# Kernel tuning notes

Hardware: AMD Instinct MI355X
Metric: run time of the kernel (lower is better)

The kernel has to match this reference:

```python
import jax, jax.numpy as jnp
import numpy as np

D_MODEL = 1024
N_HEADS = 16
DEPTH = D_MODEL // N_HEADS
D_FF = 4096
B, S = 2, 2048
EPS = 1e-5


def _layernorm(x, g, b):
    mu = jnp.mean(x, axis=-1, keepdims=True)
    var = jnp.mean(jnp.square(x - mu), axis=-1, keepdims=True)
    return (x - mu) * jax.lax.rsqrt(var + EPS) * g + b


def setup_inputs() -> dict:
    key = jax.random.key(0)
    ks = jax.random.split(key, 16)
    sd = 0.02
    d = {
        'x': jax.random.normal(ks[0], (B, S, D_MODEL), dtype=jnp.float32),
        'mask': jnp.ones((B, S), dtype=jnp.int32),
        'wq_w': jax.random.normal(ks[1], (D_MODEL, D_MODEL), dtype=jnp.float32) * sd,
        'wq_b': jnp.zeros((D_MODEL,), dtype=jnp.float32),
        'wk_w': jax.random.normal(ks[2], (D_MODEL, D_MODEL), dtype=jnp.float32) * sd,
        'wk_b': jnp.zeros((D_MODEL,), dtype=jnp.float32),
        'wv_w': jax.random.normal(ks[3], (D_MODEL, D_MODEL), dtype=jnp.float32) * sd,
        'wv_b': jnp.zeros((D_MODEL,), dtype=jnp.float32),
        'wo_w': jax.random.normal(ks[4], (D_MODEL, D_MODEL), dtype=jnp.float32) * sd,
        'wo_b': jnp.zeros((D_MODEL,), dtype=jnp.float32),
        'ffn_w1': jax.random.normal(ks[5], (D_MODEL, D_FF), dtype=jnp.float32) * sd,
        'ffn_b1': jnp.zeros((D_FF,), dtype=jnp.float32),
        'ffn_w2': jax.random.normal(ks[6], (D_FF, D_MODEL), dtype=jnp.float32) * sd,
        'ffn_b2': jnp.zeros((D_MODEL,), dtype=jnp.float32),
        'ln1_g': jnp.ones((D_MODEL,), dtype=jnp.float32),
        'ln1_b': jnp.zeros((D_MODEL,), dtype=jnp.float32),
        'ln2_g': jnp.ones((D_MODEL,), dtype=jnp.float32),
        'ln2_b': jnp.zeros((D_MODEL,), dtype=jnp.float32),
    }
    return d


def reference(x, mask, wq_w, wq_b, wk_w, wk_b, wv_w, wv_b, wo_w, wo_b,
              ffn_w1, ffn_b1, ffn_w2, ffn_b2, ln1_g, ln1_b, ln2_g, ln2_b):
    b, s, _ = x.shape
    # projections [B,S,D] -> [B,H,S,depth]
    def split_heads(t):
        return t.reshape(b, s, N_HEADS, DEPTH).transpose(0, 2, 1, 3)
    q = split_heads(x @ wq_w + wq_b)
    k = split_heads(x @ wk_w + wk_b)
    v = split_heads(x @ wv_w + wv_b)
    # scores [B,H,S,S]
    logits = jnp.einsum('bhqd,bhkd->bhqk', q, k) / jnp.sqrt(jnp.float32(DEPTH))
    m = mask[:, None, None, :]  # [B,1,1,S] broadcast over heads/query
    logits = jnp.where(m == 0, jnp.float32(-1e9), logits)
    attn = jax.nn.softmax(logits, axis=-1)
    ctx = jnp.einsum('bhqk,bhkd->bhqd', attn, v)
    ctx = ctx.transpose(0, 2, 1, 3).reshape(b, s, D_MODEL)
    attn_out = ctx @ wo_w + wo_b
    out1 = _layernorm(x + attn_out, ln1_g, ln1_b)
    ffn = jax.nn.relu(out1 @ ffn_w1 + ffn_b1) @ ffn_w2 + ffn_b2
    out2 = _layernorm(out1 + ffn, ln2_g, ln2_b)
    return out2
```

## Files before the change

kernel.cpp:

```cpp
#include <hip/hip_runtime.h>
#include <hip/hip_bf16.h>

#define D_MODEL 1024
#define N_HEADS 16
#define DEPTH   64
#define D_FF    4096
#define BATCH   2
#define SEQ     2048
#define NTOK    (BATCH * SEQ)
#define EPS     1e-5f

typedef __attribute__((ext_vector_type(8))) short short8;
typedef __attribute__((ext_vector_type(4))) float f32x4;
typedef __attribute__((ext_vector_type(4))) unsigned short ushort4v;
typedef __attribute__((ext_vector_type(8))) unsigned short ushort8v;

__device__ __forceinline__ unsigned short f2bf(float f) {
    union { __hip_bfloat16 h; unsigned short u; } cv;
    cv.h = __float2bfloat16(f);
    return cv.u;
}

__device__ __forceinline__ float bf2f(unsigned short u) {
    union { float f; unsigned int i; } c;
    c.i = (unsigned int)u << 16;
    return c.f;
}

__device__ __forceinline__ float exp2_fast(float x) {
    float r;
    asm("v_exp_f32 %0, %1" : "=v"(r) : "v"(x));
    return r;
}

__device__ __forceinline__ void gload16(const unsigned short* g, unsigned short* lds) {
    __builtin_amdgcn_global_load_lds(
        (const __attribute__((address_space(1))) void*)g,
        (__attribute__((address_space(3))) void*)lds, 16, 0, 0);
}

__device__ __forceinline__ void tc_tile(
    const float* __restrict__ W, unsigned short* __restrict__ WT,
    int K, int N, int bn64, int bk64, int tid, float (*t)[65])
{
    const int bk = bk64 * 64, bn = bn64 * 64;
    const int c4 = tid & 15, r0 = tid >> 4;
#pragma unroll
    for (int i = 0; i < 4; ++i) {
        int k = r0 + i * 16;
        f32x4 v = *(const f32x4*)&W[(size_t)(bk + k) * N + bn + c4 * 4];
#pragma unroll
        for (int jj = 0; jj < 4; ++jj) t[k][c4 * 4 + jj] = v[jj];
    }
    __syncthreads();
#pragma unroll
    for (int i = 0; i < 4; ++i) {
        int n = r0 + i * 16;
        ushort4v o;
#pragma unroll
        for (int jj = 0; jj < 4; ++jj) o[jj] = f2bf(t[c4 * 4 + jj][n]);
        *(ushort4v*)&WT[(size_t)(bn + n) * K + bk + c4 * 4] = o;
    }
}

__global__ __launch_bounds__(256) void prep_kernel(
    const float* __restrict__ wq_w, const float* __restrict__ wk_w,
    const float* __restrict__ wv_w, const float* __restrict__ wo_w,
    const float* __restrict__ ffn_w1, const float* __restrict__ ffn_w2,
    const float* __restrict__ wq_b, const float* __restrict__ wk_b,
    const float* __restrict__ wv_b, const float* __restrict__ x,
    unsigned short* __restrict__ wqkvT, unsigned short* __restrict__ woT,
    unsigned short* __restrict__ w1T, unsigned short* __restrict__ w2T,
    float* __restrict__ biasqkv, unsigned short* __restrict__ actb)
{
    __shared__ float t[64][65];
    const int idx = blockIdx.x, tid = threadIdx.x;

    if (idx < 1024) {
        const int wsel = idx >> 8, rel = idx & 255;
        const float* W = (wsel == 0) ? wq_w : (wsel == 1) ? wk_w : (wsel == 2) ? wv_w : wo_w;
        unsigned short* WT = (wsel == 3) ? woT : (wqkvT + (size_t)wsel * 1024 * 1024);
        tc_tile(W, WT, 1024, 1024, rel & 15, rel >> 4, tid, t);
    } else if (idx < 2048) {
        const int rel = idx - 1024;
        tc_tile(ffn_w1, w1T, 1024, 4096, rel & 63, rel >> 6, tid, t);
    } else if (idx < 3072) {
        const int rel = idx - 2048;
        tc_tile(ffn_w2, w2T, 4096, 1024, rel & 15, rel >> 4, tid, t);
    } else if (idx < 3084) {
        const int i = (idx - 3072) * 256 + tid;
        if (i < 1024) biasqkv[i] = wq_b[i];
        else if (i < 2048) biasqkv[i] = wk_b[i - 1024];
        else if (i < 3072) biasqkv[i] = wv_b[i - 2048];
    } else {
        const int i = ((idx - 3084) * 256 + tid) * 8;
        f32x4 a = *(const f32x4*)&x[i];
        f32x4 b = *(const f32x4*)&x[i + 4];
        ushort8v o;
        o[0] = f2bf(a[0]); o[1] = f2bf(a[1]); o[2] = f2bf(a[2]); o[3] = f2bf(a[3]);
        o[4] = f2bf(b[0]); o[5] = f2bf(b[1]); o[6] = f2bf(b[2]); o[7] = f2bf(b[3]);
        *(ushort8v*)&actb[i] = o;
    }
}

__global__ __launch_bounds__(256) void vtrans_kernel(
    const unsigned short* __restrict__ QKV, unsigned short* __restrict__ Vt)
{
    __shared__ unsigned short T[64][72];
    const int st = blockIdx.x * 64;
    const int h = blockIdx.y, b = blockIdx.z;
    const int tid = threadIdx.x;
    const size_t tok0 = (size_t)b * SEQ;
    const int LD = 3 * D_MODEL;
    const int r = tid >> 3, c8 = (tid & 7) * 8;
#pragma unroll
    for (int p = 0; p < 2; ++p) {
        int row = p * 32 + r;
        *(ushort8v*)&T[row][c8] =
            *(const ushort8v*)&QKV[(tok0 + st + row) * LD + 2048 + h * 64 + c8];
    }
    __syncthreads();
    const int bh = b * N_HEADS + h;
#pragma unroll
    for (int p = 0; p < 2; ++p) {
        int d = p * 32 + r;
        ushort8v o;
#pragma unroll
        for (int e = 0; e < 8; ++e) o[e] = T[c8 + e][d];
        *(ushort8v*)&Vt[((size_t)bh * 64 + d) * SEQ + st + c8] = o;
    }
}

__global__ __launch_bounds__(512, 2) void gemm256_kernel(
    const unsigned short* __restrict__ A, const unsigned short* __restrict__ BT,
    const float* __restrict__ bias, float* __restrict__ C,
    unsigned short* __restrict__ Cb,
    int M, int N, int lda, int kLen, int ksplit, int relu, int out_bf)
{
    __shared__ unsigned short As[2][256 * 64];
    __shared__ unsigned short Bs[2][256 * 64];
    const int tid = threadIdx.x;
    const int lane = tid & 63, w = tid >> 6;
    const int wr = w >> 2, wc = w & 3;
    const int lr = lane & 15, g = lane >> 4;

    const int nwg = gridDim.x;
    int wg = blockIdx.x;
    if ((nwg & 7) == 0) wg = (wg & 7) * (nwg >> 3) + (wg >> 3);
    if (ksplit > 1) {
        const int ntile = nwg / ksplit;
        const int split = wg / ntile;
        wg = wg % ntile;
        A  += (size_t)split * kLen;
        BT += (size_t)split * kLen;
        C  += (size_t)split * M * N;
        Cb += (size_t)split * M * N;
    }
    const int gx = N >> 8;
    const int bm = (wg / gx) * 256, bn = (wg % gx) * 256;

    const int srow = (w << 3) + (lane >> 3);
    const int scol = ((lane & 7) ^ (lane >> 3)) << 3;
    const int ldst = (w << 9);

#define STG(P, Xs, bufi, hf, rb, k0)                                            \
    {                                                                            \
        gload16(P + (size_t)((rb) + (hf) * 128 + srow) * lda + (k0) + scol,      \
                &Xs[bufi][(hf) * 8192 + ldst]);                                  \
        gload16(P + (size_t)((rb) + (hf) * 128 + 64 + srow) * lda + (k0) + scol, \
                &Xs[bufi][(hf) * 8192 + 4096 + ldst]);                           \
    }

    const int NS = kLen >> 6;
    f32x4 acc[8][4] = {};

    STG(A,  As, 0, 0, bm, 0); STG(A,  As, 0, 1, bm, 0);
    STG(BT, Bs, 0, 0, bn, 0); STG(BT, Bs, 0, 1, bn, 0);
    if (NS > 1) { STG(BT, Bs, 1, 0, bn, 64); STG(BT, Bs, 1, 1, bn, 64); }
    asm volatile("s_waitcnt vmcnt(4)" ::: "memory");
    __builtin_amdgcn_s_barrier();
    asm volatile("" ::: "memory");

    int buf = 0;
    short8 af[4][2], b0[2][2], b1[2][2];
    for (int s = 0; s < NS; ++s) {
        const int kn1 = (s + 1) << 6, kn2 = (s + 2) << 6;

#pragma unroll
        for (int i = 0; i < 4; ++i)
#pragma unroll
            for (int kk = 0; kk < 2; ++kk)
                af[i][kk] = *(const short8*)&As[buf][(wr * 128 + i * 16 + lr) * 64
                                                    + (((kk * 4 + g) ^ (lr & 7)) << 3)];
#pragma unroll
        for (int j = 0; j < 2; ++j)
#pragma unroll
            for (int kk = 0; kk < 2; ++kk)
                b0[j][kk] = *(const short8*)&Bs[buf][(wc * 64 + j * 16 + lr) * 64
                                                    + (((kk * 4 + g) ^ (lr & 7)) << 3)];
        if (s + 1 < NS) STG(A, As, buf ^ 1, 0, bm, kn1);
        asm volatile("" ::: "memory");
        __builtin_amdgcn_s_barrier();
        asm volatile("" ::: "memory");
        __builtin_amdgcn_s_setprio(1);
#pragma unroll
        for (int i = 0; i < 4; ++i)
#pragma unroll
            for (int j = 0; j < 2; ++j) {
                acc[i][j] = __builtin_amdgcn_mfma_f32_16x16x32_bf16(af[i][0], b0[j][0], acc[i][j], 0, 0, 0);
                acc[i][j] = __builtin_amdgcn_mfma_f32_16x16x32_bf16(af[i][1], b0[j][1], acc[i][j], 0, 0, 0);
            }
        __builtin_amdgcn_s_setprio(0);
        asm volatile("" ::: "memory");
        __builtin_amdgcn_s_barrier();
        asm volatile("" ::: "memory");

#pragma unroll
        for (int j = 0; j < 2; ++j)
#pragma unroll
            for (int kk = 0; kk < 2; ++kk)
                b1[j][kk] = *(const short8*)&Bs[buf][(wc * 64 + (j + 2) * 16 + lr) * 64
                                                    + (((kk * 4 + g) ^ (lr & 7)) << 3)];
        if (s + 1 < NS) STG(A, As, buf ^ 1, 1, bm, kn1);
        asm volatile("" ::: "memory");
        __builtin_amdgcn_s_barrier();
        asm volatile("" ::: "memory");
        __builtin_amdgcn_s_setprio(1);
#pragma unroll
        for (int i = 0; i < 4; ++i)
#pragma unroll
            for (int j = 0; j < 2; ++j) {
                acc[i][j + 2] = __builtin_amdgcn_mfma_f32_16x16x32_bf16(af[i][0], b1[j][0], acc[i][j + 2], 0, 0, 0);
                acc[i][j + 2] = __builtin_amdgcn_mfma_f32_16x16x32_bf16(af[i][1], b1[j][1], acc[i][j + 2], 0, 0, 0);
            }
        __builtin_amdgcn_s_setprio(0);
        asm volatile("" ::: "memory");
        __builtin_amdgcn_s_barrier();
        asm volatile("" ::: "memory");

#pragma unroll
        for (int i = 0; i < 4; ++i)
#pragma unroll
            for (int kk = 0; kk < 2; ++kk)
                af[i][kk] = *(const short8*)&As[buf][(wr * 128 + 64 + i * 16 + lr) * 64
                                                    + (((kk * 4 + g) ^ (lr & 7)) << 3)];
        if (s + 2 < NS) STG(BT, Bs, buf, 0, bn, kn2);
        asm volatile("" ::: "memory");
        __builtin_amdgcn_s_barrier();
        asm volatile("" ::: "memory");
        __builtin_amdgcn_s_setprio(1);
#pragma unroll
        for (int i = 0; i < 4; ++i)
#pragma unroll
            for (int j = 0; j < 2; ++j) {
                acc[i + 4][j] = __builtin_amdgcn_mfma_f32_16x16x32_bf16(af[i][0], b0[j][0], acc[i + 4][j], 0, 0, 0);
                acc[i + 4][j] = __builtin_amdgcn_mfma_f32_16x16x32_bf16(af[i][1], b0[j][1], acc[i + 4][j], 0, 0, 0);
            }
        __builtin_amdgcn_s_setprio(0);
        asm volatile("" ::: "memory");
        __builtin_amdgcn_s_barrier();
        asm volatile("" ::: "memory");

        if (s + 2 < NS) STG(BT, Bs, buf, 1, bn, kn2);
        asm volatile("" ::: "memory");
        __builtin_amdgcn_s_barrier();
        asm volatile("" ::: "memory");
        __builtin_amdgcn_s_setprio(1);
#pragma unroll
        for (int i = 0; i < 4; ++i)
#pragma unroll
            for (int j = 0; j < 2; ++j) {
                acc[i + 4][j + 2] = __builtin_amdgcn_mfma_f32_16x16x32_bf16(af[i][0], b1[j][0], acc[i + 4][j + 2], 0, 0, 0);
                acc[i + 4][j + 2] = __builtin_amdgcn_mfma_f32_16x16x32_bf16(af[i][1], b1[j][1], acc[i + 4][j + 2], 0, 0, 0);
            }
        __builtin_amdgcn_s_setprio(0);
        asm volatile("s_waitcnt vmcnt(4)" ::: "memory");
        __builtin_amdgcn_s_barrier();
        asm volatile("" ::: "memory");

        buf ^= 1;
    }
#undef STG

#pragma unroll
    for (int i = 0; i < 8; ++i)
#pragma unroll
        for (int j = 0; j < 4; ++j) {
            const int col = bn + wc * 64 + j * 16 + lr;
            const float bv = bias ? bias[col] : 0.f;
#pragma unroll
            for (int r = 0; r < 4; ++r) {
                const int row = bm + wr * 128 + i * 16 + g * 4 + r;
                float v = acc[i][j][r] + bv;
                if (relu) v = fmaxf(v, 0.f);
                if (out_bf) Cb[(size_t)row * N + col] = f2bf(v);
                else        C [(size_t)row * N + col] = v;
            }
        }
}

__global__ __launch_bounds__(256) void gemm_bt_kernel(
    const unsigned short* __restrict__ A, const unsigned short* __restrict__ BT,
    const float* __restrict__ bias, float* __restrict__ C,
    unsigned short* __restrict__ Cb,
    int M, int N, int lda, int kLen, int relu, int out_bf)
{
    __shared__ unsigned short As[128 * 64];
    __shared__ unsigned short Bs[128 * 64];
    const int tid = threadIdx.x;
    const int lane = tid & 63, wv = tid >> 6;
    const int wr = wv >> 1, wc = wv & 1;
    const int bm = blockIdx.y * 128, bn = blockIdx.x * 128;
    const int kbase = blockIdx.z * kLen;
    const int lr = lane & 15, lk = (lane >> 4) << 3;

    C  += (size_t)blockIdx.z * M * N;
    Cb += (size_t)blockIdx.z * M * N;

    f32x4 acc[4][4] = {};

    for (int kt = 0; kt < kLen; kt += 64) {
#pragma unroll
        for (int c = 0; c < 4; ++c) {
            int e = c * 2048 + tid * 8;
            int row = e >> 6, k = e & 63;
            gload16(A  + (size_t)(bm + row) * lda + kbase + kt + k, As + c * 2048 + wv * 512);
            gload16(BT + (size_t)(bn + row) * lda + kbase + kt + k, Bs + c * 2048 + wv * 512);
        }
        __syncthreads();
#pragma unroll
        for (int kk = 0; kk < 2; ++kk) {
            short8 af[4], bfr[4];
#pragma unroll
            for (int i = 0; i < 4; ++i) {
                af[i]  = *(const short8*)&As[(wr * 64 + i * 16 + lr) * 64 + kk * 32 + lk];
                bfr[i] = *(const short8*)&Bs[(wc * 64 + i * 16 + lr) * 64 + kk * 32 + lk];
            }
#pragma unroll
            for (int i = 0; i < 4; ++i)
#pragma unroll
                for (int j = 0; j < 4; ++j)
                    acc[i][j] = __builtin_amdgcn_mfma_f32_16x16x32_bf16(
                        af[i], bfr[j], acc[i][j], 0, 0, 0);
        }
        __syncthreads();
    }

    const int r0 = bm + wr * 64, c0 = bn + wc * 64;
    const int rq = (lane >> 4) * 4;
#pragma unroll
    for (int i = 0; i < 4; ++i)
#pragma unroll
        for (int j = 0; j < 4; ++j) {
            int col = c0 + j * 16 + lr;
            float bv = bias ? bias[col] : 0.f;
#pragma unroll
            for (int r = 0; r < 4; ++r) {
                int row = r0 + i * 16 + rq + r;
                float v = acc[i][j][r] + bv;
                if (relu) v = fmaxf(v, 0.f);
                if (out_bf) Cb[(size_t)row * N + col] = f2bf(v);
                else        C [(size_t)row * N + col] = v;
            }
        }
}

__global__ __launch_bounds__(256, 3) void attn_mfma_kernel(
    const unsigned short* __restrict__ QKV,
    const unsigned short* __restrict__ Vt,
    const int* __restrict__ mask,
    unsigned short* __restrict__ Op, float* __restrict__ mA, float* __restrict__ lA)
{
    const int tid = threadIdx.x;
    const int lane = tid & 63, w = tid >> 6;
    const int lr = lane & 15, g = lane >> 4;
    const int qt = blockIdx.x * 128;
    const int h = blockIdx.y;
    const int b = blockIdx.z >> 1, sp = blockIdx.z & 1;
    const int bh = b * N_HEADS + h;
    const size_t tok0 = (size_t)b * SEQ;
    const int kvb0 = sp * (SEQ / 2);
    const int LD = 3 * D_MODEL;
    const float C1 = 0.18033688f;

    __shared__ unsigned short Ks[2][64 * 64];
    __shared__ unsigned short Vs[2][64 * 64];
    __shared__ unsigned short Ps[4][32 * 64];
    __shared__ float Msk[2][64];

    short8 onesB;
#pragma unroll
    for (int e = 0; e < 8; ++e) onesB[e] = (short)0x3F80;

    short8 qf[2][2];
#pragma unroll
    for (int i = 0; i < 2; ++i)
#pragma unroll
        for (int kk = 0; kk < 2; ++kk)
            qf[i][kk] = *(const short8*)&QKV[(tok0 + qt + w * 32 + i * 16 + lr) * LD
                                             + h * 64 + kk * 32 + g * 8];

    const int rsub = w * 8 + (lane >> 3);
    const int slot = lane & 7;

    float m_[2] = {20.f, 20.f};
    f32x4 lacc[2] = {};
    f32x4 o_[2][4] = {};

    {
#pragma unroll
        for (int p = 0; p < 2; ++p) {
            const int row = p * 32 + rsub;
            const int ss = slot ^ (row & 7);
            gload16(QKV + (tok0 + kvb0 + row) * LD + D_MODEL + h * 64 + ss * 8,
                    &Ks[0][(p * 32 + w * 8) * 64]);
            gload16(Vt + ((size_t)bh * 64 + row) * SEQ + kvb0 + ss * 8,
                    &Vs[0][(p * 32 + w * 8) * 64]);
        }
        if (tid < 64) Msk[0][tid] = mask[b * SEQ + kvb0 + tid] ? 0.f : -1e9f;
    }
    __syncthreads();

    const int NT = (SEQ / 2) / 64;
    int buf = 0;
    for (int t = 0; t < NT; ++t) {
        if (t + 1 < NT) {
            const int nb = buf ^ 1;
            const int kvn = kvb0 + (t + 1) * 64;
#pragma unroll
            for (int p = 0; p < 2; ++p) {
                const int row = p * 32 + rsub;
                const int ss = slot ^ (row & 7);
                gload16(QKV + (tok0 + kvn + row) * LD + D_MODEL + h * 64 + ss * 8,
                        &Ks[nb][(p * 32 + w * 8) * 64]);
                gload16(Vt + ((size_t)bh * 64 + row) * SEQ + kvn + ss * 8,
                        &Vs[nb][(p * 32 + w * 8) * 64]);
            }
            if (tid < 64) Msk[nb][tid] = mask[b * SEQ + kvn + tid] ? 0.f : -1e9f;
        }

        f32x4 sacc[2][4] = {};
#pragma unroll
        for (int j = 0; j < 4; ++j) {
            short8 kf0 = *(const short8*)&Ks[buf][(j * 16 + lr) * 64 + ((0 + g) ^ (lr & 7)) * 8];
            short8 kf1 = *(const short8*)&Ks[buf][(j * 16 + lr) * 64 + ((4 + g) ^ (lr & 7)) * 8];
#pragma unroll
            for (int i = 0; i < 2; ++i) {
                sacc[i][j] = __builtin_amdgcn_mfma_f32_16x16x32_bf16(kf0, qf[i][0], sacc[i][j], 0, 0, 0);
                sacc[i][j] = __builtin_amdgcn_mfma_f32_16x16x32_bf16(kf1, qf[i][1], sacc[i][j], 0, 0, 0);
            }
        }

        float mb[4][4];
#pragma unroll
        for (int j = 0; j < 4; ++j) {
            f32x4 mrow = *(const f32x4*)&Msk[buf][j * 16 + g * 4];
#pragma unroll
            for (int r = 0; r < 4; ++r) mb[j][r] = mrow[r];
        }

        float tmv[2];
#pragma unroll
        for (int i = 0; i < 2; ++i) {
            float x[4][4];
            float tm = -1e30f;
#pragma unroll
            for (int j = 0; j < 4; ++j)
#pragma unroll
                for (int r = 0; r < 4; ++r) {
                    x[j][r] = fmaf(sacc[i][j][r], C1, mb[j][r]);
                    tm = fmaxf(tm, x[j][r]);
                }
#pragma unroll
            for (int j = 0; j < 4; ++j) {
                ushort4v pw;
#pragma unroll
                for (int r = 0; r < 4; ++r)
                    pw[r] = f2bf(exp2_fast(x[j][r] - m_[i]));
                *(ushort4v*)((char*)&Ps[w][0] + (i * 16 + lr) * 128
                             + ((j * 32 + g * 8) ^ ((lr & 7) << 4))) = pw;
            }
            tm = fmaxf(tm, __shfl_xor(tm, 16));
            tm = fmaxf(tm, __shfl_xor(tm, 32));
            tmv[i] = tm;
        }

#pragma unroll
        for (int kk = 0; kk < 2; ++kk) {
            short8 pf[2];
#pragma unroll
            for (int i = 0; i < 2; ++i) {
                pf[i] = *(const short8*)&Ps[w][(i * 16 + lr) * 64 + ((kk * 4 + g) ^ (lr & 7)) * 8];
                lacc[i] = __builtin_amdgcn_mfma_f32_16x16x32_bf16(pf[i], onesB, lacc[i], 0, 0, 0);
            }
#pragma unroll
            for (int dj = 0; dj < 4; ++dj) {
                short8 vf = *(const short8*)&Vs[buf][(dj * 16 + lr) * 64 + ((kk * 4 + g) ^ (lr & 7)) * 8];
#pragma unroll
                for (int i = 0; i < 2; ++i)
                    o_[i][dj] = __builtin_amdgcn_mfma_f32_16x16x32_bf16(pf[i], vf, o_[i][dj], 0, 0, 0);
            }
        }

#pragma unroll
        for (int i = 0; i < 2; ++i) {
            if (__any(tmv[i] > m_[i] + 8.f)) {
                const float nm = fmaxf(m_[i], tmv[i]);
                const float sc = exp2_fast(m_[i] - nm);
                m_[i] = nm;
#pragma unroll
                for (int r = 0; r < 4; ++r) {
                    const float s_r = __shfl(sc, g * 4 + r);
                    lacc[i][r] *= s_r;
#pragma unroll
                    for (int dj = 0; dj < 4; ++dj) o_[i][dj][r] *= s_r;
                }
            }
        }

        __syncthreads();
        buf ^= 1;
    }

    const int rowbase = (sp * 32 + bh) * 2048;
#pragma unroll
    for (int i = 0; i < 2; ++i) {
#pragma unroll
        for (int r = 0; r < 4; ++r) {
            const int q = qt + w * 32 + i * 16 + g * 4 + r;
            unsigned short* op = Op + (size_t)(rowbase + q) * 64;
#pragma unroll
            for (int dj = 0; dj < 4; ++dj) op[dj * 16 + lr] = f2bf(o_[i][dj][r]);
        }
        if (g == 0) mA[rowbase + qt + w * 32 + i * 16 + lr] = m_[i];
        if (lr == 0) {
#pragma unroll
            for (int r = 0; r < 4; ++r)
                lA[rowbase + qt + w * 32 + i * 16 + g * 4 + r] = lacc[i][r];
        }
    }
}

__global__ __launch_bounds__(256) void attn_merge_kernel(
    const unsigned short* __restrict__ Op, const float* __restrict__ mA,
    const float* __restrict__ lA, unsigned short* __restrict__ ctx)
{
    const int tid = threadIdx.x;
    const int row = blockIdx.x * 16 + (tid >> 4);
    const int d4 = (tid & 15) * 4;
    const int bh = row >> 11, q = row & 2047;
    const int b = bh >> 4, h = bh & 15;
    const float m0 = mA[row], m1 = mA[65536 + row];
    const float l0 = lA[row], l1 = lA[65536 + row];
    const float m = fmaxf(m0, m1);
    const float a0 = exp2_fast(m0 - m), a1 = exp2_fast(m1 - m);
    const float inv = 1.f / (l0 * a0 + l1 * a1);
    ushort4v O0 = *(const ushort4v*)&Op[(size_t)row * 64 + d4];
    ushort4v O1 = *(const ushort4v*)&Op[((size_t)65536 + row) * 64 + d4];
    ushort4v o;
#pragma unroll
    for (int e = 0; e < 4; ++e)
        o[e] = f2bf((bf2f(O0[e]) * a0 + bf2f(O1[e]) * a1) * inv);
    *(ushort4v*)&ctx[((size_t)(b * SEQ + q)) * D_MODEL + h * 64 + d4] = o;
}

__global__ __launch_bounds__(256) void reduce_ln_kernel(
    const void* __restrict__ P, int pbf, int nsplit, const float* __restrict__ bias,
    const float* __restrict__ X, const float* __restrict__ g,
    const float* __restrict__ be, float* __restrict__ out,
    unsigned short* __restrict__ outb)
{
    const int row = blockIdx.x, tid = threadIdx.x;
    __shared__ float red[4];
    const size_t MN = (size_t)NTOK * D_MODEL;
    const size_t base = (size_t)row * D_MODEL + tid * 4;

    f32x4 s = *(const f32x4*)(X + base);
    f32x4 bb = *(const f32x4*)(bias + tid * 4);
    s += bb;
    if (pbf) {
        const unsigned short* Pb = (const unsigned short*)P;
        for (int sp = 0; sp < nsplit; ++sp) {
            ushort4v pv = *(const ushort4v*)(Pb + sp * MN + base);
#pragma unroll
            for (int e = 0; e < 4; ++e) s[e] += bf2f(pv[e]);
        }
    } else {
        const float* Pf = (const float*)P;
        for (int sp = 0; sp < nsplit; ++sp)
            s += *(const f32x4*)(Pf + sp * MN + base);
    }

    float ls = s[0] + s[1] + s[2] + s[3];
#pragma unroll
    for (int o = 32; o > 0; o >>= 1) ls += __shfl_down(ls, o);
    if ((tid & 63) == 0) red[tid >> 6] = ls;
    __syncthreads();
    const float mu = (red[0] + red[1] + red[2] + red[3]) * (1.f / D_MODEL);
    __syncthreads();

    float d0 = s[0] - mu, d1 = s[1] - mu, d2 = s[2] - mu, d3 = s[3] - mu;
    float lv = d0 * d0 + d1 * d1 + d2 * d2 + d3 * d3;
#pragma unroll
    for (int o = 32; o > 0; o >>= 1) lv += __shfl_down(lv, o);
    if ((tid & 63) == 0) red[tid >> 6] = lv;
    __syncthreads();
    const float var = (red[0] + red[1] + red[2] + red[3]) * (1.f / D_MODEL);
    const float inv = rsqrtf(var + EPS);

    f32x4 gv = *(const f32x4*)(g + tid * 4);
    f32x4 bv = *(const f32x4*)(be + tid * 4);
    f32x4 o4 = {d0 * inv * gv[0] + bv[0], d1 * inv * gv[1] + bv[1],
                d2 * inv * gv[2] + bv[2], d3 * inv * gv[3] + bv[3]};
    *(f32x4*)(out + base) = o4;
    if (outb) {
        ushort4v ob = {f2bf(o4[0]), f2bf(o4[1]), f2bf(o4[2]), f2bf(o4[3])};
        *(ushort4v*)(outb + base) = ob;
    }
}

extern "C" void kernel_launch(void* const* d_in, const int* in_sizes, int n_in,
                              void* d_out, int out_size, void* d_ws, size_t ws_size,
                              hipStream_t stream) {
    const float* x      = (const float*)d_in[0];
    const int*   mask   = (const int*)  d_in[1];
    const float* wq_w   = (const float*)d_in[2];
    const float* wq_b   = (const float*)d_in[3];
    const float* wk_w   = (const float*)d_in[4];
    const float* wk_b   = (const float*)d_in[5];
    const float* wv_w   = (const float*)d_in[6];
    const float* wv_b   = (const float*)d_in[7];
    const float* wo_w   = (const float*)d_in[8];
    const float* wo_b   = (const float*)d_in[9];
    const float* ffn_w1 = (const float*)d_in[10];
    const float* ffn_b1 = (const float*)d_in[11];
    const float* ffn_w2 = (const float*)d_in[12];
    const float* ffn_b2 = (const float*)d_in[13];
    const float* ln1_g  = (const float*)d_in[14];
    const float* ln1_b  = (const float*)d_in[15];
    const float* ln2_g  = (const float*)d_in[16];
    const float* ln2_b  = (const float*)d_in[17];
    float* out = (float*)d_out;

    char* w = (char*)d_ws;
    const size_t MB = 1024 * 1024;
    unsigned short* actb    = (unsigned short*)(w);
    unsigned short* wqkvT   = (unsigned short*)(w + 8 * MB);
    float*          biasqkv = (float*)(w + 14 * MB);
    unsigned short* qkvb    = (unsigned short*)(w + 16 * MB);
    unsigned short* vt      = (unsigned short*)(w + 40 * MB);
    unsigned short* ctxb    = (unsigned short*)(w + 48 * MB);
    unsigned short* Opb     = (unsigned short*)(w + 56 * MB);
    float*          mAb     = (float*)(w + 72 * MB);
    float*          lAb     = (float*)(w + 73 * MB);
    unsigned short* woT     = (unsigned short*)(w + 74 * MB);
    unsigned short* woPb    = (unsigned short*)(w);
    float*          Out1    = (float*)(w + 64 * MB);
    unsigned short* out1b   = (unsigned short*)(w + 40 * MB);
    unsigned short* fhb     = (unsigned short*)(w + 80 * MB);
    unsigned short* w2T     = (unsigned short*)(w + 112 * MB);
    unsigned short* w1T     = (unsigned short*)(w + 120 * MB);
    unsigned short* f2Pb    = (unsigned short*)(w);

    dim3 blk(256);

    prep_kernel<<<dim3(5132), blk, 0, stream>>>(
        wq_w, wk_w, wv_w, wo_w, ffn_w1, ffn_w2, wq_b, wk_b, wv_b, x,
        wqkvT, woT, w1T, w2T, biasqkv, actb);

    gemm256_kernel<<<dim3(192), dim3(512), 0, stream>>>(actb, wqkvT, biasqkv, nullptr, qkvb,
                                                        NTOK, 3072, 1024, 1024, 1, 0, 1);
    vtrans_kernel<<<dim3(SEQ / 64, N_HEADS, BATCH), blk, 0, stream>>>(qkvb, vt);

    attn_mfma_kernel<<<dim3(SEQ / 128, N_HEADS, BATCH * 2), blk, 0, stream>>>(
        qkvb, vt, mask, Opb, mAb, lAb);
    attn_merge_kernel<<<dim3((BATCH * N_HEADS * SEQ) / 16), blk, 0, stream>>>(
        Opb, mAb, lAb, ctxb);

    gemm_bt_kernel<<<dim3(8, 32, 2), blk, 0, stream>>>(ctxb, woT, nullptr, nullptr, woPb,
                                                       NTOK, 1024, 1024, 512, 0, 1);
    reduce_ln_kernel<<<dim3(NTOK), blk, 0, stream>>>(woPb, 1, 2, wo_b, x, ln1_g, ln1_b,
                                                     Out1, out1b);
    gemm256_kernel<<<dim3(256), dim3(512), 0, stream>>>(out1b, w1T, ffn_b1, nullptr, fhb,
                                                        NTOK, D_FF, 1024, 1024, 1, 1, 1);
    gemm256_kernel<<<dim3(256), dim3(512), 0, stream>>>(fhb, w2T, nullptr, nullptr, f2Pb,
                                                        NTOK, 1024, 4096, 1024, 4, 0, 1);
    reduce_ln_kernel<<<dim3(NTOK), blk, 0, stream>>>(f2Pb, 1, 4, ffn_b2, Out1, ln2_g, ln2_b,
                                                     out, nullptr);
}
```

Baseline: 248.3 us.

## Single-buffer attention K/V in LDS with register prefetch for higher occupancy

The attention kernel drops the double-buffered LDS tiles for K, V and mask and prefetches the next tile into registers via global loads. After compute, the registers are written to a single LDS buffer, which costs a second barrier per iteration. Launch bounds rise from 3 to 4 blocks per CU, since LDS use per block falls. The trade is more VGPR pressure and an extra sync against higher occupancy.

```diff
diff --git a/kernel.cpp b/kernel.cpp
--- a/kernel.cpp
+++ b/kernel.cpp
@@ -365,7 +365,7 @@
         }
 }
 
-__global__ __launch_bounds__(256, 3) void attn_mfma_kernel(
+__global__ __launch_bounds__(256, 4) void attn_mfma_kernel(
     const unsigned short* __restrict__ QKV,
     const unsigned short* __restrict__ Vt,
     const int* __restrict__ mask,
@@ -383,10 +383,10 @@
     const int LD = 3 * D_MODEL;
     const float C1 = 0.18033688f;
 
-    __shared__ unsigned short Ks[2][64 * 64];
-    __shared__ unsigned short Vs[2][64 * 64];
+    __shared__ unsigned short Ks[64 * 64];
+    __shared__ unsigned short Vs[64 * 64];
     __shared__ unsigned short Ps[4][32 * 64];
-    __shared__ float Msk[2][64];
+    __shared__ float Msk[64];
 
     short8 onesB;
 #pragma unroll
@@ -402,48 +402,53 @@
 
     const int rsub = w * 8 + (lane >> 3);
     const int slot = lane & 7;
+    int wofs[2];
+#pragma unroll
+    for (int p = 0; p < 2; ++p) {
+        const int row = p * 32 + rsub;
+        wofs[p] = row * 64 + ((slot ^ (row & 7)) << 3);
+    }
 
     float m_[2] = {20.f, 20.f};
     f32x4 lacc[2] = {};
     f32x4 o_[2][4] = {};
 
-    {
-#pragma unroll
-        for (int p = 0; p < 2; ++p) {
-            const int row = p * 32 + rsub;
-            const int ss = slot ^ (row & 7);
-            gload16(QKV + (tok0 + kvb0 + row) * LD + D_MODEL + h * 64 + ss * 8,
-                    &Ks[0][(p * 32 + w * 8) * 64]);
-            gload16(Vt + ((size_t)bh * 64 + row) * SEQ + kvb0 + ss * 8,
-                    &Vs[0][(p * 32 + w * 8) * 64]);
-        }
-        if (tid < 64) Msk[0][tid] = mask[b * SEQ + kvb0 + tid] ? 0.f : -1e9f;
-    }
+    ushort8v kreg[2], vreg[2];
+    int mreg = 1;
+
+#pragma unroll
+    for (int p = 0; p < 2; ++p) {
+        const int row = p * 32 + rsub;
+        kreg[p] = *(const ushort8v*)&QKV[(tok0 + kvb0 + row) * LD + D_MODEL + h * 64 + slot * 8];
+        vreg[p] = *(const ushort8v*)&Vt[((size_t)bh * 64 + row) * SEQ + kvb0 + slot * 8];
+    }
+    if (tid < 64) mreg = mask[b * SEQ + kvb0 + tid];
+#pragma unroll
+    for (int p = 0; p < 2; ++p) {
+        *(ushort8v*)&Ks[wofs[p]] = kreg[p];
+        *(ushort8v*)&Vs[wofs[p]] = vreg[p];
+    }
+    if (tid < 64) Msk[tid] = mreg ? 0.f : -1e9f;
     __syncthreads();
 
     const int NT = (SEQ / 2) / 64;
-    int buf = 0;
     for (int t = 0; t < NT; ++t) {
         if (t + 1 < NT) {
-            const int nb = buf ^ 1;
             const int kvn = kvb0 + (t + 1) * 64;
 #pragma unroll
             for (int p = 0; p < 2; ++p) {
                 const int row = p * 32 + rsub;
-                const int ss = slot ^ (row & 7);
-                gload16(QKV + (tok0 + kvn + row) * LD + D_MODEL + h * 64 + ss * 8,
-                        &Ks[nb][(p * 32 + w * 8) * 64]);
-                gload16(Vt + ((size_t)bh * 64 + row) * SEQ + kvn + ss * 8,
-                        &Vs[nb][(p * 32 + w * 8) * 64]);
-            }
-            if (tid < 64) Msk[nb][tid] = mask[b * SEQ + kvn + tid] ? 0.f : -1e9f;
+                kreg[p] = *(const ushort8v*)&QKV[(tok0 + kvn + row) * LD + D_MODEL + h * 64 + slot * 8];
+                vreg[p] = *(const ushort8v*)&Vt[((size_t)bh * 64 + row) * SEQ + kvn + slot * 8];
+            }
+            if (tid < 64) mreg = mask[b * SEQ + kvn + tid];
         }
 
         f32x4 sacc[2][4] = {};
 #pragma unroll
         for (int j = 0; j < 4; ++j) {
-            short8 kf0 = *(const short8*)&Ks[buf][(j * 16 + lr) * 64 + ((0 + g) ^ (lr & 7)) * 8];
-            short8 kf1 = *(const short8*)&Ks[buf][(j * 16 + lr) * 64 + ((4 + g) ^ (lr & 7)) * 8];
+            short8 kf0 = *(const short8*)&Ks[(j * 16 + lr) * 64 + ((0 + g) ^ (lr & 7)) * 8];
+            short8 kf1 = *(const short8*)&Ks[(j * 16 + lr) * 64 + ((4 + g) ^ (lr & 7)) * 8];
 #pragma unroll
             for (int i = 0; i < 2; ++i) {
                 sacc[i][j] = __builtin_amdgcn_mfma_f32_16x16x32_bf16(kf0, qf[i][0], sacc[i][j], 0, 0, 0);
@@ -454,7 +459,7 @@
         float mb[4][4];
 #pragma unroll
         for (int j = 0; j < 4; ++j) {
-            f32x4 mrow = *(const f32x4*)&Msk[buf][j * 16 + g * 4];
+            f32x4 mrow = *(const f32x4*)&Msk[j * 16 + g * 4];
 #pragma unroll
             for (int r = 0; r < 4; ++r) mb[j][r] = mrow[r];
         }
@@ -495,7 +500,7 @@
             }
 #pragma unroll
             for (int dj = 0; dj < 4; ++dj) {
-                short8 vf = *(const short8*)&Vs[buf][(dj * 16 + lr) * 64 + ((kk * 4 + g) ^ (lr & 7)) * 8];
+                short8 vf = *(const short8*)&Vs[(dj * 16 + lr) * 64 + ((kk * 4 + g) ^ (lr & 7)) * 8];
 #pragma unroll
                 for (int i = 0; i < 2; ++i)
                     o_[i][dj] = __builtin_amdgcn_mfma_f32_16x16x32_bf16(pf[i], vf, o_[i][dj], 0, 0, 0);
@@ -519,7 +524,16 @@
         }
 
         __syncthreads();
-        buf ^= 1;
+
+        if (t + 1 < NT) {
+#pragma unroll
+            for (int p = 0; p < 2; ++p) {
+                *(ushort8v*)&Ks[wofs[p]] = kreg[p];
+                *(ushort8v*)&Vs[wofs[p]] = vreg[p];
+            }
+            if (tid < 64) Msk[tid] = mreg ? 0.f : -1e9f;
+        }
+        __syncthreads();
     }
 
     const int rowbase = (sp * 32 + bh) * 2048;
```

New measurement: 316.7 us. +27.5%, slower.

## Process 256 query rows per attention block to reuse staged K/V tiles

Applied to the files above, without the earlier changes.

Each attention workgroup now handles two 128-row query halves, reusing every K/V tile loaded into shared memory for both halves. The grid shrinks by half and the occupancy hint drops from 3 to 2 blocks per CU to make room for the doubled Q fragments and accumulators. This halves global K/V traffic and the per-tile sync overhead. The cost is higher register pressure, fewer blocks in flight (512 total), and possibly less latency hiding.

```diff
diff --git a/kernel.cpp b/kernel.cpp
--- a/kernel.cpp
+++ b/kernel.cpp
@@ -365,7 +365,7 @@
         }
 }
 
-__global__ __launch_bounds__(256, 3) void attn_mfma_kernel(
+__global__ __launch_bounds__(256, 2) void attn_mfma_kernel(
     const unsigned short* __restrict__ QKV,
     const unsigned short* __restrict__ Vt,
     const int* __restrict__ mask,
@@ -374,7 +374,7 @@
     const int tid = threadIdx.x;
     const int lane = tid & 63, w = tid >> 6;
     const int lr = lane & 15, g = lane >> 4;
-    const int qt = blockIdx.x * 128;
+    const int qt = blockIdx.x * 256;
     const int h = blockIdx.y;
     const int b = blockIdx.z >> 1, sp = blockIdx.z & 1;
     const int bh = b * N_HEADS + h;
@@ -392,20 +392,23 @@
 #pragma unroll
     for (int e = 0; e < 8; ++e) onesB[e] = (short)0x3F80;
 
-    short8 qf[2][2];
-#pragma unroll
-    for (int i = 0; i < 2; ++i)
-#pragma unroll
-        for (int kk = 0; kk < 2; ++kk)
-            qf[i][kk] = *(const short8*)&QKV[(tok0 + qt + w * 32 + i * 16 + lr) * LD
-                                             + h * 64 + kk * 32 + g * 8];
+    short8 qf[2][2][2];
+#pragma unroll
+    for (int hf = 0; hf < 2; ++hf)
+#pragma unroll
+        for (int i = 0; i < 2; ++i)
+#pragma unroll
+            for (int kk = 0; kk < 2; ++kk)
+                qf[hf][i][kk] = *(const short8*)&QKV[
+                    (tok0 + qt + hf * 128 + w * 32 + i * 16 + lr) * LD
+                    + h * 64 + kk * 32 + g * 8];
 
     const int rsub = w * 8 + (lane >> 3);
     const int slot = lane & 7;
 
-    float m_[2] = {20.f, 20.f};
-    f32x4 lacc[2] = {};
-    f32x4 o_[2][4] = {};
+    float m_[2][2] = {{20.f, 20.f}, {20.f, 20.f}};
+    f32x4 lacc[2][2] = {};
+    f32x4 o_[2][2][4] = {};
 
     {
 #pragma unroll
@@ -439,18 +442,6 @@
             if (tid < 64) Msk[nb][tid] = mask[b * SEQ + kvn + tid] ? 0.f : -1e9f;
         }
 
-        f32x4 sacc[2][4] = {};
-#pragma unroll
-        for (int j = 0; j < 4; ++j) {
-            short8 kf0 = *(const short8*)&Ks[buf][(j * 16 + lr) * 64 + ((0 + g) ^ (lr & 7)) * 8];
-            short8 kf1 = *(const short8*)&Ks[buf][(j * 16 + lr) * 64 + ((4 + g) ^ (lr & 7)) * 8];
-#pragma unroll
-            for (int i = 0; i < 2; ++i) {
-                sacc[i][j] = __builtin_amdgcn_mfma_f32_16x16x32_bf16(kf0, qf[i][0], sacc[i][j], 0, 0, 0);
-                sacc[i][j] = __builtin_amdgcn_mfma_f32_16x16x32_bf16(kf1, qf[i][1], sacc[i][j], 0, 0, 0);
-            }
-        }
-
         float mb[4][4];
 #pragma unroll
         for (int j = 0; j < 4; ++j) {
@@ -459,61 +450,76 @@
             for (int r = 0; r < 4; ++r) mb[j][r] = mrow[r];
         }
 
-        float tmv[2];
-#pragma unroll
-        for (int i = 0; i < 2; ++i) {
-            float x[4][4];
-            float tm = -1e30f;
-#pragma unroll
-            for (int j = 0; j < 4; ++j)
-#pragma unroll
-                for (int r = 0; r < 4; ++r) {
-                    x[j][r] = fmaf(sacc[i][j][r], C1, mb[j][r]);
-                    tm = fmaxf(tm, x[j][r]);
+#pragma unroll
+        for (int hf = 0; hf < 2; ++hf) {
+            f32x4 sacc[2][4] = {};
+#pragma unroll
+            for (int j = 0; j < 4; ++j) {
+                short8 kf0 = *(const short8*)&Ks[buf][(j * 16 + lr) * 64 + ((0 + g) ^ (lr & 7)) * 8];
+                short8 kf1 = *(const short8*)&Ks[buf][(j * 16 + lr) * 64 + ((4 + g) ^ (lr & 7)) * 8];
+#pragma unroll
+                for (int i = 0; i < 2; ++i) {
+                    sacc[i][j] = __builtin_amdgcn_mfma_f32_16x16x32_bf16(kf0, qf[hf][i][0], sacc[i][j], 0, 0, 0);
+                    sacc[i][j] = __builtin_amdgcn_mfma_f32_16x16x32_bf16(kf1, qf[hf][i][1], sacc[i][j], 0, 0, 0);
                 }
-#pragma unroll
-            for (int j = 0; j < 4; ++j) {
-                ushort4v pw;
-#pragma unroll
-                for (int r = 0; r < 4; ++r)
-                    pw[r] = f2bf(exp2_fast(x[j][r] - m_[i]));
-                *(ushort4v*)((char*)&Ps[w][0] + (i * 16 + lr) * 128
-                             + ((j * 32 + g * 8) ^ ((lr & 7) << 4))) = pw;
-            }
-            tm = fmaxf(tm, __shfl_xor(tm, 16));
-            tm = fmaxf(tm, __shfl_xor(tm, 32));
-            tmv[i] = tm;
-        }
-
-#pragma unroll
-        for (int kk = 0; kk < 2; ++kk) {
-            short8 pf[2];
+            }
+
+            float tmv[2];
 #pragma unroll
             for (int i = 0; i < 2; ++i) {
-                pf[i] = *(const short8*)&Ps[w][(i * 16 + lr) * 64 + ((kk * 4 + g) ^ (lr & 7)) * 8];
-                lacc[i] = __builtin_amdgcn_mfma_f32_16x16x32_bf16(pf[i], onesB, lacc[i], 0, 0, 0);
-            }
-#pragma unroll
-            for (int dj = 0; dj < 4; ++dj) {
-                short8 vf = *(const short8*)&Vs[buf][(dj * 16 + lr) * 64 + ((kk * 4 + g) ^ (lr & 7)) * 8];
-#pragma unroll
-                for (int i = 0; i < 2; ++i)
-                    o_[i][dj] = __builtin_amdgcn_mfma_f32_16x16x32_bf16(pf[i], vf, o_[i][dj], 0, 0, 0);
-            }
-        }
-
-#pragma unroll
-        for (int i = 0; i < 2; ++i) {
-            if (__any(tmv[i] > m_[i] + 8.f)) {
-                const float nm = fmaxf(m_[i], tmv[i]);
-                const float sc = exp2_fast(m_[i] - nm);
-                m_[i] = nm;
-#pragma unroll
-                for (int r = 0; r < 4; ++r) {
-                    const float s_r = __shfl(sc, g * 4 + r);
-                    lacc[i][r] *= s_r;
-#pragma unroll
-                    for (int dj = 0; dj < 4; ++dj) o_[i][dj][r] *= s_r;
+                float x[4][4];
+                float tm = -1e30f;
+#pragma unroll
+                for (int j = 0; j < 4; ++j)
+#pragma unroll
+                    for (int r = 0; r < 4; ++r) {
+                        x[j][r] = fmaf(sacc[i][j][r], C1, mb[j][r]);
+                        tm = fmaxf(tm, x[j][r]);
+                    }
+#pragma unroll
+                for (int j = 0; j < 4; ++j) {
+                    ushort4v pw;
+#pragma unroll
+                    for (int r = 0; r < 4; ++r)
+                        pw[r] = f2bf(exp2_fast(x[j][r] - m_[hf][i]));
+                    *(ushort4v*)((char*)&Ps[w][0] + (i * 16 + lr) * 128
+                                 + ((j * 32 + g * 8) ^ ((lr & 7) << 4))) = pw;
+                }
+                tm = fmaxf(tm, __shfl_xor(tm, 16));
+                tm = fmaxf(tm, __shfl_xor(tm, 32));
+                tmv[i] = tm;
+            }
+
+#pragma unroll
+            for (int kk = 0; kk < 2; ++kk) {
+                short8 pf[2];
+#pragma unroll
+                for (int i = 0; i < 2; ++i) {
+                    pf[i] = *(const short8*)&Ps[w][(i * 16 + lr) * 64 + ((kk * 4 + g) ^ (lr & 7)) * 8];
+                    lacc[hf][i] = __builtin_amdgcn_mfma_f32_16x16x32_bf16(pf[i], onesB, lacc[hf][i], 0, 0, 0);
+                }
+#pragma unroll
+                for (int dj = 0; dj < 4; ++dj) {
+                    short8 vf = *(const short8*)&Vs[buf][(dj * 16 + lr) * 64 + ((kk * 4 + g) ^ (lr & 7)) * 8];
+#pragma unroll
+                    for (int i = 0; i < 2; ++i)
+                        o_[hf][i][dj] = __builtin_amdgcn_mfma_f32_16x16x32_bf16(pf[i], vf, o_[hf][i][dj], 0, 0, 0);
+                }
+            }
+
+#pragma unroll
+            for (int i = 0; i < 2; ++i) {
+                if (__any(tmv[i] > m_[hf][i] + 8.f)) {
+                    const float nm = fmaxf(m_[hf][i], tmv[i]);
+                    const float sc = exp2_fast(m_[hf][i] - nm);
+                    m_[hf][i] = nm;
+#pragma unroll
+                    for (int r = 0; r < 4; ++r) {
+                        const float s_r = __shfl(sc, g * 4 + r);
+                        lacc[hf][i][r] *= s_r;
+#pragma unroll
+                        for (int dj = 0; dj < 4; ++dj) o_[hf][i][dj][r] *= s_r;
+                    }
                 }
             }
         }
@@ -524,21 +530,24 @@
 
     const int rowbase = (sp * 32 + bh) * 2048;
 #pragma unroll
-    for (int i = 0; i < 2; ++i) {
-#pragma unroll
-        for (int r = 0; r < 4; ++r) {
-            const int q = qt + w * 32 + i * 16 + g * 4 + r;
-            unsigned short* op = Op + (size_t)(rowbase + q) * 64;
-#pragma unroll
-            for (int dj = 0; dj < 4; ++dj) op[dj * 16 + lr] = f2bf(o_[i][dj][r]);
-        }
-        if (g == 0) mA[rowbase + qt + w * 32 + i * 16 + lr] = m_[i];
-        if (lr == 0) {
-#pragma unroll
-            for (int r = 0; r < 4; ++r)
-                lA[rowbase + qt + w * 32 + i * 16 + g * 4 + r] = lacc[i][r];
-        }
-    }
+    for (int hf = 0; hf < 2; ++hf)
+#pragma unroll
+        for (int i = 0; i < 2; ++i) {
+            const int qb = qt + hf * 128 + w * 32 + i * 16;
+#pragma unroll
+            for (int r = 0; r < 4; ++r) {
+                const int q = qb + g * 4 + r;
+                unsigned short* op = Op + (size_t)(rowbase + q) * 64;
+#pragma unroll
+                for (int dj = 0; dj < 4; ++dj) op[dj * 16 + lr] = f2bf(o_[hf][i][dj][r]);
+            }
+            if (g == 0) mA[rowbase + qb + lr] = m_[hf][i];
+            if (lr == 0) {
+#pragma unroll
+                for (int r = 0; r < 4; ++r)
+                    lA[rowbase + qb + g * 4 + r] = lacc[hf][i][r];
+            }
+        }
 }
 
 __global__ __launch_bounds__(256) void attn_merge_kernel(
@@ -672,7 +681,7 @@
                                                         NTOK, 3072, 1024, 1024, 1, 0, 1);
     vtrans_kernel<<<dim3(SEQ / 64, N_HEADS, BATCH), blk, 0, stream>>>(qkvb, vt);
 
-    attn_mfma_kernel<<<dim3(SEQ / 128, N_HEADS, BATCH * 2), blk, 0, stream>>>(
+    attn_mfma_kernel<<<dim3(SEQ / 256, N_HEADS, BATCH * 2), blk, 0, stream>>>(
         qkvb, vt, mask, Opb, mAb, lAb);
     attn_merge_kernel<<<dim3((BATCH * N_HEADS * SEQ) / 16), blk, 0, stream>>>(
         Opb, mAb, lAb, ctxb);
```

New measurement: 244.2 us. No clear change (-1.7%).
